# Performance work log

Measured on AMD Instinct MI355X. Metric: run time of the kernel, lower is better.

Reference implementation:

```python
import jax, jax.numpy as jnp
import numpy as np

WS = 7          # window size
NH = 16         # n_heads
DIM = 512
HEAD_DIM = DIM // NH
SCALE = HEAD_DIM ** -0.5


def _rel_pos_index(ws):
    coords = np.stack(np.meshgrid(np.arange(ws), np.arange(ws), indexing='ij'))  # [2,ws,ws]
    coords = coords.reshape(2, -1)                                               # [2,N]
    rel = coords[:, :, None] - coords[:, None, :]                                # [2,N,N]
    idx = (rel[0] + ws - 1) * (2 * ws - 1) + (rel[1] + ws - 1)                   # [N,N]
    return jnp.asarray(idx, dtype=jnp.int32)


def _window_partition(x, ws):
    B, H, W, C = x.shape
    x = x.reshape(B, H // ws, ws, W // ws, ws, C)
    x = x.transpose(0, 1, 3, 2, 4, 5)
    return x.reshape(-1, ws * ws, C)  # [B*nW, N, C]


def setup_inputs() -> dict:
    key = jax.random.key(0)
    k1, k2, k3 = jax.random.split(key, 3)
    qkv = jax.random.normal(k1, (3, 32, 56, 56, DIM), dtype=jnp.float32)
    mask = jax.random.normal(k2, (64, WS * WS, WS * WS), dtype=jnp.float32)
    bias_table = jax.random.normal(k3, ((2 * WS - 1) ** 2, NH), dtype=jnp.float32) * 0.02
    return {"qkv": qkv, "mask": mask, "bias_table": bias_table}


def reference(qkv, mask, bias_table):
    q, k, v = qkv[0], qkv[1], qkv[2]
    B, H, W, C = q.shape
    N = WS * WS
    # window partition + split heads -> [BS, NH, N, HEAD_DIM]
    def prep(x):
        x = _window_partition(x, WS)                       # [BS, N, C]
        BS = x.shape[0]
        return x.reshape(BS, N, NH, HEAD_DIM).transpose(0, 2, 1, 3)
    q, k, v = prep(q), prep(k), prep(v)
    BS = q.shape[0]

    attn = jnp.einsum('bhnd,bhmd->bhnm', q, k) * SCALE      # [BS, NH, N, N]

    idx = _rel_pos_index(WS)                                # [N, N] static
    rel_bias = bias_table[idx]                              # [N, N, NH]
    attn = attn + rel_bias.transpose(2, 0, 1)[None]         # [BS, NH, N, N]

    nW = mask.shape[0]
    attn = attn.reshape(BS // nW, nW, NH, N, N) + mask[None, :, None]
    attn = attn.reshape(BS, NH, N, N)

    attn = jax.nn.softmax(attn, axis=-1)
    x = jnp.einsum('bhnm,bhmd->bhnd', attn, v)              # [BS, NH, N, HEAD_DIM]
    return x.transpose(0, 2, 1, 3).reshape(BS, N, C)
```

## Files before the change

### kernel.cpp

```cpp
#include <hip/hip_runtime.h>

#define NTOK 49
#define NH 16
#define DIM 512
#define HD 32
#define HPB 4
#define SCALE 0.17677669529663687f
#define NEGINF -3.0e38f

typedef __attribute__((ext_vector_type(8))) short short8;
typedef __attribute__((ext_vector_type(16))) float f32x16;
typedef __attribute__((ext_vector_type(2))) unsigned uint2v;

struct __attribute__((packed, aligned(4))) f4u { float x, y, z, w; };

__device__ __forceinline__ unsigned short fb(float x) {
    return __builtin_bit_cast(unsigned short, (__bf16)x);
}

__device__ __forceinline__ float b2f(unsigned short b) {
    union { unsigned u; float f; } v; v.u = ((unsigned)b) << 16;
    return v.f;
}

__device__ __forceinline__ unsigned long long pk4(float4 v) {
    unsigned lo = (unsigned)fb(v.x) | ((unsigned)fb(v.y) << 16);
    unsigned hi = (unsigned)fb(v.z) | ((unsigned)fb(v.w) << 16);
    return (unsigned long long)lo | ((unsigned long long)hi << 32);
}

__device__ __forceinline__ short8 pk8s(float4 a, float4 b, float sc) {
    short8 r;
    r[0] = (short)fb(a.x * sc); r[1] = (short)fb(a.y * sc);
    r[2] = (short)fb(a.z * sc); r[3] = (short)fb(a.w * sc);
    r[4] = (short)fb(b.x * sc); r[5] = (short)fb(b.y * sc);
    r[6] = (short)fb(b.z * sc); r[7] = (short)fb(b.w * sc);
    return r;
}

__device__ __forceinline__ uint2v xhalf(unsigned W) {
    return __builtin_amdgcn_permlane32_swap(W, W, false, false);
}

__global__ __launch_bounds__(256, 5) void winattn_mfma(
    const float* __restrict__ qkv,
    const float* __restrict__ mask,
    const float* __restrict__ bias_table,
    float* __restrict__ out)
{
    __shared__ __align__(16) unsigned short Vr[HPB][64][32];
    __shared__ __align__(8)  unsigned short maskw[2404];
    __shared__ float biasw[HPB][176];
    __shared__ float invl[HPB][64];

    const int bx   = blockIdx.x;
    const int win  = bx >> 2;
    const int hg   = bx & 3;
    const int tid  = threadIdx.x;
    const int wave = tid >> 6;
    const int lane = tid & 63;
    const int ln   = lane & 31;
    const int h    = lane >> 5;
    const int head = hg * HPB + wave;
    const int hs   = h * 16;

    const int b  = win >> 6;
    const int w  = win & 63;
    const int wr = w >> 3, wc = w & 7;

    const size_t plane = (size_t)32 * 56 * 56 * 512;
    const size_t wbase = (((size_t)(b * 56 + wr * 7)) * 56 + wc * 7) * 512 + head * HD;

    const float* mrow = mask + (size_t)w * 2401;
    for (int e = tid; e < 600; e += 256) {
        f4u mv = *(const f4u*)(mrow + 4 * e);
        unsigned long long pk =
              (unsigned long long)fb(mv.x)
            | ((unsigned long long)fb(mv.y) << 16)
            | ((unsigned long long)fb(mv.z) << 32)
            | ((unsigned long long)fb(mv.w) << 48);
        *(unsigned long long*)&maskw[4 * e] = pk;
    }
    if (tid == 0) maskw[2400] = fb(mrow[2400]);

    const int t0 = ln;
    const int t1 = (32 + ln <= 48) ? (32 + ln) : 48;
    float4 qv[2][4], kv[2][4];
    #pragma unroll
    for (int tt = 0; tt < 2; ++tt) {
        const int t  = tt ? t1 : t0;
        const int i  = t / 7, j = t - i * 7;
        const float* qp = qkv + wbase + (size_t)(i * 56 + j) * 512 + h * 8;
        const float* kp = qp + plane;
        qv[tt][0] = *(const float4*)(qp);
        qv[tt][1] = *(const float4*)(qp + 4);
        qv[tt][2] = *(const float4*)(qp + 16);
        qv[tt][3] = *(const float4*)(qp + 20);
        kv[tt][0] = *(const float4*)(kp);
        kv[tt][1] = *(const float4*)(kp + 4);
        kv[tt][2] = *(const float4*)(kp + 16);
        kv[tt][3] = *(const float4*)(kp + 20);
    }

    #pragma unroll
    for (int e = 0; e < 8; ++e) {
        const int idx = e * 64 + lane;
        const int t   = idx >> 3;
        const int d4  = idx & 7;
        unsigned long long vz = 0;
        if (t < NTOK) {
            const int i = t / 7, j = t - i * 7;
            vz = pk4(*(const float4*)(qkv + 2 * plane + wbase
                                      + (size_t)(i * 56 + j) * 512 + d4 * 4));
        }
        *(unsigned long long*)&Vr[wave][t][d4 * 4] = vz;
    }

    for (int r = lane; r < 169; r += 64)
        biasw[wave][r] = bias_table[r * NH + head];

    short8 qfr[2][2], kfr[2][2];
    #pragma unroll
    for (int tt = 0; tt < 2; ++tt) {
        qfr[tt][0] = pk8s(qv[tt][0], qv[tt][1], SCALE);
        qfr[tt][1] = pk8s(qv[tt][2], qv[tt][3], SCALE);
        kfr[tt][0] = pk8s(kv[tt][0], kv[tt][1], 1.0f);
        kfr[tt][1] = pk8s(kv[tt][2], kv[tt][3], 1.0f);
    }

    f32x16 zer;
    #pragma unroll
    for (int i = 0; i < 16; ++i) zer[i] = 0.f;
    f32x16 acc[2][2];
    acc[0][0] = zer; acc[0][1] = zer; acc[1][0] = zer; acc[1][1] = zer;
    #pragma unroll
    for (int ks = 0; ks < 2; ++ks) {
        acc[0][0] = __builtin_amdgcn_mfma_f32_32x32x16_bf16(kfr[0][ks], qfr[0][ks], acc[0][0], 0, 0, 0);
        acc[0][1] = __builtin_amdgcn_mfma_f32_32x32x16_bf16(kfr[0][ks], qfr[1][ks], acc[0][1], 0, 0, 0);
        acc[1][0] = __builtin_amdgcn_mfma_f32_32x32x16_bf16(kfr[1][ks], qfr[0][ks], acc[1][0], 0, 0, 0);
        acc[1][1] = __builtin_amdgcn_mfma_f32_32x32x16_bf16(kfr[1][ks], qfr[1][ks], acc[1][1], 0, 0, 0);
    }

    __syncthreads();

    unsigned wpk[2][2][8];
    #pragma unroll
    for (int nt = 0; nt < 2; ++nt) {
        const int n  = 32 * nt + ln;
        const int nc = n < NTOK ? n : NTOK - 1;
        const int i_n = nc / 7;
        const int tn  = nc + 6 * i_n + 84;
        float sum = 0.f;
        #pragma unroll
        for (int mt = 0; mt < 2; ++mt) {
            #pragma unroll
            for (int g = 0; g < 8; ++g) {
                const int ia = (g < 4) ? g : g + 4;
                float e0, e1;
                {
                    const int mb  = 32 * mt + (ia & 3) + 8 * (ia >> 2);
                    const int m0  = mb, m1 = mb + 4;
                    const int mc0 = m0 < NTOK ? m0 : NTOK - 1;
                    const int mc1 = m1 < NTOK ? m1 : NTOK - 1;
                    const int tm0 = mc0 + 6 * (mc0 / 7);
                    const int tm1 = mc1 + 6 * (mc1 / 7);
                    const int mc  = h ? mc1 : mc0;
                    const int tm  = h ? tm1 : tm0;
                    float s = acc[mt][nt][ia] + biasw[wave][tn - tm]
                            + b2f(maskw[nc * NTOK + mc]);
                    const bool dead = h ? (m1 >= NTOK) : (m0 >= NTOK);
                    e0 = __expf(dead ? NEGINF : s);
                }
                {
                    const int rb  = ia + 4;
                    const int mb  = 32 * mt + (rb & 3) + 8 * (rb >> 2);
                    const int m0  = mb, m1 = mb + 4;
                    if (m0 >= NTOK && m1 >= NTOK) {
                        e1 = 0.f;
                    } else {
                        const int mc0 = m0 < NTOK ? m0 : NTOK - 1;
                        const int mc1 = m1 < NTOK ? m1 : NTOK - 1;
                        const int tm0 = mc0 + 6 * (mc0 / 7);
                        const int tm1 = mc1 + 6 * (mc1 / 7);
                        const int mc  = h ? mc1 : mc0;
                        const int tm  = h ? tm1 : tm0;
                        float s = acc[mt][nt][rb] + biasw[wave][tn - tm]
                                + b2f(maskw[nc * NTOK + mc]);
                        const bool dead = h ? (m1 >= NTOK) : (m0 >= NTOK);
                        e1 = __expf(dead ? NEGINF : s);
                    }
                }
                sum += e0 + e1;
                wpk[nt][mt][g] = (unsigned)fb(e0) | ((unsigned)fb(e1) << 16);
            }
        }
        {
            const uint2v ss = xhalf(__builtin_bit_cast(unsigned, sum));
            const unsigned so = h ? ss[0] : ss[1];
            sum += __builtin_bit_cast(float, so);
        }
        if (h == 0 && n < NTOK)
            invl[wave][n] = 1.0f / sum;
    }

    f32x16 oacc[2];
    oacc[0] = zer; oacc[1] = zer;
    #pragma unroll
    for (int ksv = 0; ksv < 4; ++ksv) {
        short8 vf;
        #pragma unroll
        for (int j = 0; j < 8; ++j)
            vf[j] = (short)Vr[wave][16 * ksv + 8 * h + j][ln];
        const int mt = ksv >> 1;
        #pragma unroll
        for (int nt = 0; nt < 2; ++nt) {
            short8 af;
            #pragma unroll
            for (int jj = 0; jj < 4; ++jj) {
                const unsigned W = wpk[nt][mt][(ksv & 1) * 4 + jj];
                const uint2v S = xhalf(W);
                af[jj]     = (short)(unsigned short)((S[0] >> hs) & 0xffffu);
                af[jj + 4] = (short)(unsigned short)((S[1] >> hs) & 0xffffu);
            }
            oacc[nt] = __builtin_amdgcn_mfma_f32_32x32x16_bf16(af, vf, oacc[nt], 0, 0, 0);
        }
    }

    const size_t obase = ((size_t)win * NTOK) * DIM + head * HD + ln;
    #pragma unroll
    for (int nt = 0; nt < 2; ++nt) {
        #pragma unroll
        for (int r = 0; r < 16; ++r) {
            const int nb = 32 * nt + (r & 3) + 8 * (r >> 2);
            const int n  = h ? nb + 4 : nb;
            if (n < NTOK)
                out[obase + (size_t)n * DIM] = oacc[nt][r] * invl[wave][n];
        }
    }
}

extern "C" void kernel_launch(void* const* d_in, const int* in_sizes, int n_in,
                              void* d_out, int out_size, void* d_ws, size_t ws_size,
                              hipStream_t stream) {
    const float* qkv        = (const float*)d_in[0];
    const float* mask       = (const float*)d_in[1];
    const float* bias_table = (const float*)d_in[2];
    float* out = (float*)d_out;

    winattn_mfma<<<2048 * 4, 256, 0, stream>>>(qkv, mask, bias_table, out);
}
```

Before: 208.4 us.

## Split each head's query tiles across two waves, doubling block count

Each block now handles two heads instead of four, and the two query row tiles of a head go to separate waves. Each wave loads only its own Q tile, runs half the QK and PV MFMAs, and holds fewer accumulators, which cuts register pressure and per-wave latency. The cost is that K, V, the mask and the bias are each loaded and converted twice per head, and twice as many blocks are launched, so global and LDS staging traffic goes up.

Result: slower. 215.2 us (+3.2%).

```diff
diff --git a/kernel.cpp b/kernel.cpp
--- a/kernel.cpp
+++ b/kernel.cpp
@@ -4,7 +4,6 @@
 #define NH 16
 #define DIM 512
 #define HD 32
-#define HPB 4
 #define SCALE 0.17677669529663687f
 #define NEGINF -3.0e38f
 
@@ -42,26 +41,27 @@
     return __builtin_amdgcn_permlane32_swap(W, W, false, false);
 }
 
-__global__ __launch_bounds__(256, 5) void winattn_mfma(
+__global__ __launch_bounds__(256, 5) void winattn_split(
     const float* __restrict__ qkv,
     const float* __restrict__ mask,
     const float* __restrict__ bias_table,
     float* __restrict__ out)
 {
-    __shared__ __align__(16) unsigned short Vr[HPB][64][32];
+    __shared__ __align__(16) unsigned short Vr[4][64][32];
     __shared__ __align__(8)  unsigned short maskw[2404];
-    __shared__ float biasw[HPB][176];
-    __shared__ float invl[HPB][64];
+    __shared__ float biasw[4][176];
+    __shared__ float invl[4][64];
 
     const int bx   = blockIdx.x;
-    const int win  = bx >> 2;
-    const int hg   = bx & 3;
+    const int win  = bx >> 3;
+    const int hg   = bx & 7;
     const int tid  = threadIdx.x;
     const int wave = tid >> 6;
     const int lane = tid & 63;
     const int ln   = lane & 31;
     const int h    = lane >> 5;
-    const int head = hg * HPB + wave;
+    const int head = hg * 2 + (wave >> 1);
+    const int ntw  = wave & 1;
     const int hs   = h * 16;
 
     const int b  = win >> 6;
@@ -85,21 +85,25 @@
 
     const int t0 = ln;
     const int t1 = (32 + ln <= 48) ? (32 + ln) : 48;
-    float4 qv[2][4], kv[2][4];
+    const int tq = ntw ? t1 : t0;
+    float4 kv[2][4], qv[4];
     #pragma unroll
     for (int tt = 0; tt < 2; ++tt) {
         const int t  = tt ? t1 : t0;
         const int i  = t / 7, j = t - i * 7;
-        const float* qp = qkv + wbase + (size_t)(i * 56 + j) * 512 + h * 8;
-        const float* kp = qp + plane;
-        qv[tt][0] = *(const float4*)(qp);
-        qv[tt][1] = *(const float4*)(qp + 4);
-        qv[tt][2] = *(const float4*)(qp + 16);
-        qv[tt][3] = *(const float4*)(qp + 20);
+        const float* kp = qkv + plane + wbase + (size_t)(i * 56 + j) * 512 + h * 8;
         kv[tt][0] = *(const float4*)(kp);
         kv[tt][1] = *(const float4*)(kp + 4);
         kv[tt][2] = *(const float4*)(kp + 16);
         kv[tt][3] = *(const float4*)(kp + 20);
+    }
+    {
+        const int i = tq / 7, j = tq - i * 7;
+        const float* qp = qkv + wbase + (size_t)(i * 56 + j) * 512 + h * 8;
+        qv[0] = *(const float4*)(qp);
+        qv[1] = *(const float4*)(qp + 4);
+        qv[2] = *(const float4*)(qp + 16);
+        qv[3] = *(const float4*)(qp + 20);
     }
 
     #pragma unroll
@@ -119,34 +123,30 @@
     for (int r = lane; r < 169; r += 64)
         biasw[wave][r] = bias_table[r * NH + head];
 
-    short8 qfr[2][2], kfr[2][2];
-    #pragma unroll
-    for (int tt = 0; tt < 2; ++tt) {
-        qfr[tt][0] = pk8s(qv[tt][0], qv[tt][1], SCALE);
-        qfr[tt][1] = pk8s(qv[tt][2], qv[tt][3], SCALE);
-        kfr[tt][0] = pk8s(kv[tt][0], kv[tt][1], 1.0f);
-        kfr[tt][1] = pk8s(kv[tt][2], kv[tt][3], 1.0f);
-    }
+    short8 qfr[2], kfr[2][2];
+    qfr[0]    = pk8s(qv[0], qv[1], SCALE);
+    qfr[1]    = pk8s(qv[2], qv[3], SCALE);
+    kfr[0][0] = pk8s(kv[0][0], kv[0][1], 1.0f);
+    kfr[0][1] = pk8s(kv[0][2], kv[0][3], 1.0f);
+    kfr[1][0] = pk8s(kv[1][0], kv[1][1], 1.0f);
+    kfr[1][1] = pk8s(kv[1][2], kv[1][3], 1.0f);
 
     f32x16 zer;
     #pragma unroll
     for (int i = 0; i < 16; ++i) zer[i] = 0.f;
-    f32x16 acc[2][2];
-    acc[0][0] = zer; acc[0][1] = zer; acc[1][0] = zer; acc[1][1] = zer;
+    f32x16 acc[2];
+    acc[0] = zer; acc[1] = zer;
     #pragma unroll
     for (int ks = 0; ks < 2; ++ks) {
-        acc[0][0] = __builtin_amdgcn_mfma_f32_32x32x16_bf16(kfr[0][ks], qfr[0][ks], acc[0][0], 0, 0, 0);
-        acc[0][1] = __builtin_amdgcn_mfma_f32_32x32x16_bf16(kfr[0][ks], qfr[1][ks], acc[0][1], 0, 0, 0);
-        acc[1][0] = __builtin_amdgcn_mfma_f32_32x32x16_bf16(kfr[1][ks], qfr[0][ks], acc[1][0], 0, 0, 0);
-        acc[1][1] = __builtin_amdgcn_mfma_f32_32x32x16_bf16(kfr[1][ks], qfr[1][ks], acc[1][1], 0, 0, 0);
+        acc[0] = __builtin_amdgcn_mfma_f32_32x32x16_bf16(kfr[0][ks], qfr[ks], acc[0], 0, 0, 0);
+        acc[1] = __builtin_amdgcn_mfma_f32_32x32x16_bf16(kfr[1][ks], qfr[ks], acc[1], 0, 0, 0);
     }
 
     __syncthreads();
 
-    unsigned wpk[2][2][8];
-    #pragma unroll
-    for (int nt = 0; nt < 2; ++nt) {
-        const int n  = 32 * nt + ln;
+    unsigned wpk[2][8];
+    {
+        const int n  = 32 * ntw + ln;
         const int nc = n < NTOK ? n : NTOK - 1;
         const int i_n = nc / 7;
         const int tn  = nc + 6 * i_n + 84;
@@ -166,7 +166,7 @@
                     const int tm1 = mc1 + 6 * (mc1 / 7);
                     const int mc  = h ? mc1 : mc0;
                     const int tm  = h ? tm1 : tm0;
-                    float s = acc[mt][nt][ia] + biasw[wave][tn - tm]
+                    float s = acc[mt][ia] + biasw[wave][tn - tm]
                             + b2f(maskw[nc * NTOK + mc]);
                     const bool dead = h ? (m1 >= NTOK) : (m0 >= NTOK);
                     e0 = __expf(dead ? NEGINF : s);
@@ -184,14 +184,14 @@
                         const int tm1 = mc1 + 6 * (mc1 / 7);
                         const int mc  = h ? mc1 : mc0;
                         const int tm  = h ? tm1 : tm0;
-                        float s = acc[mt][nt][rb] + biasw[wave][tn - tm]
+                        float s = acc[mt][rb] + biasw[wave][tn - tm]
                                 + b2f(maskw[nc * NTOK + mc]);
                         const bool dead = h ? (m1 >= NTOK) : (m0 >= NTOK);
                         e1 = __expf(dead ? NEGINF : s);
                     }
                 }
                 sum += e0 + e1;
-                wpk[nt][mt][g] = (unsigned)fb(e0) | ((unsigned)fb(e1) << 16);
+                wpk[mt][g] = (unsigned)fb(e0) | ((unsigned)fb(e1) << 16);
             }
         }
         {
@@ -200,11 +200,10 @@
             sum += __builtin_bit_cast(float, so);
         }
         if (h == 0 && n < NTOK)
-            invl[wave][n] = 1.0f / sum;
-    }
-
-    f32x16 oacc[2];
-    oacc[0] = zer; oacc[1] = zer;
+            invl[wave][ln] = 1.0f / sum;
+    }
+
+    f32x16 oacc = zer;
     #pragma unroll
     for (int ksv = 0; ksv < 4; ++ksv) {
         short8 vf;
@@ -212,30 +211,24 @@
         for (int j = 0; j < 8; ++j)
             vf[j] = (short)Vr[wave][16 * ksv + 8 * h + j][ln];
         const int mt = ksv >> 1;
+        short8 af;
         #pragma unroll
-        for (int nt = 0; nt < 2; ++nt) {
-            short8 af;
-            #pragma unroll
-            for (int jj = 0; jj < 4; ++jj) {
-                const unsigned W = wpk[nt][mt][(ksv & 1) * 4 + jj];
-                const uint2v S = xhalf(W);
-                af[jj]     = (short)(unsigned short)((S[0] >> hs) & 0xffffu);
-                af[jj + 4] = (short)(unsigned short)((S[1] >> hs) & 0xffffu);
-            }
-            oacc[nt] = __builtin_amdgcn_mfma_f32_32x32x16_bf16(af, vf, oacc[nt], 0, 0, 0);
-        }
+        for (int jj = 0; jj < 4; ++jj) {
+            const unsigned W = wpk[mt][(ksv & 1) * 4 + jj];
+            const uint2v S = xhalf(W);
+            af[jj]     = (short)(unsigned short)((S[0] >> hs) & 0xffffu);
+            af[jj + 4] = (short)(unsigned short)((S[1] >> hs) & 0xffffu);
+        }
+        oacc = __builtin_amdgcn_mfma_f32_32x32x16_bf16(af, vf, oacc, 0, 0, 0);
     }
 
     const size_t obase = ((size_t)win * NTOK) * DIM + head * HD + ln;
     #pragma unroll
-    for (int nt = 0; nt < 2; ++nt) {
-        #pragma unroll
-        for (int r = 0; r < 16; ++r) {
-            const int nb = 32 * nt + (r & 3) + 8 * (r >> 2);
-            const int n  = h ? nb + 4 : nb;
-            if (n < NTOK)
-                out[obase + (size_t)n * DIM] = oacc[nt][r] * invl[wave][n];
-        }
+    for (int r = 0; r < 16; ++r) {
+        const int nb = 32 * ntw + (r & 3) + 8 * (r >> 2);
+        const int n  = h ? nb + 4 : nb;
+        if (n < NTOK)
+            out[obase + (size_t)n * DIM] = oacc[r] * invl[wave][n - 32 * ntw];
     }
 }
 
@@ -247,5 +240,5 @@
     const float* bias_table = (const float*)d_in[2];
     float* out = (float*)d_out;
 
-    winattn_mfma<<<2048 * 4, 256, 0, stream>>>(qkv, mask, bias_table, out);
-}
+    winattn_split<<<2048 * 8, 256, 0, stream>>>(qkv, mask, bias_table, out);
+}
```
